# Kernel tuning notes

Hardware: AMD Instinct MI355X
Metric: run time of the kernel (lower is better)

The kernel has to match this reference:

```python
import jax, jax.numpy as jnp
import numpy as np
from jax import lax

B, T, D, H = 256, 512, 128, 256  # batch, seq_len, input_dim, hidden_dim


def _lstm_layer(x_seq, Wih, Whh, bih, bhh):
    """Single PyTorch-convention LSTM layer. x_seq: [B,T,Din] -> [B,T,H].
    Gate order i, f, g, o; h0 = c0 = 0."""
    Bsz = x_seq.shape[0]
    Hd = Whh.shape[1]
    # Precompute input contributions for all timesteps: [B,T,4H]
    xg = jnp.einsum('btd,gd->btg', x_seq, Wih) + bih + bhh

    def step(carry, xg_t):
        h, c = carry
        gates = xg_t + h @ Whh.T  # [B,4H]
        i, f, g, o = jnp.split(gates, 4, axis=-1)
        i = jax.nn.sigmoid(i)
        f = jax.nn.sigmoid(f)
        g = jnp.tanh(g)
        o = jax.nn.sigmoid(o)
        c = f * c + i * g
        h = o * jnp.tanh(c)
        return (h, c), h

    init = (jnp.zeros((Bsz, Hd), x_seq.dtype), jnp.zeros((Bsz, Hd), x_seq.dtype))
    _, hs = lax.scan(step, init, jnp.swapaxes(xg, 0, 1))  # hs: [T,B,H]
    return jnp.swapaxes(hs, 0, 1)


def setup_inputs() -> dict:
    key = jax.random.key(0)
    ks = jax.random.split(key, 12)
    x = jax.random.normal(ks[0], (B, T, D), dtype=jnp.float32)
    # Left-contiguous mask: lengths in [1, T] (pack_padded_sequence semantics)
    lengths = jax.random.randint(ks[1], (B,), 1, T + 1)
    mask = (jnp.arange(T)[None, :] < lengths[:, None]).astype(jnp.int32)
    s0 = 1.0 / np.sqrt(H)
    u = lambda k, shape: jax.random.uniform(k, shape, jnp.float32, -s0, s0)
    return {
        'x': x,
        'mask': mask,
        'W_ih0': u(ks[2], (4 * H, D)),
        'W_hh0': u(ks[3], (4 * H, H)),
        'b_ih0': u(ks[4], (4 * H,)),
        'b_hh0': u(ks[5], (4 * H,)),
        'W_ih1': u(ks[6], (4 * H, H)),
        'W_hh1': u(ks[7], (4 * H, H)),
        'b_ih1': u(ks[8], (4 * H,)),
        'b_hh1': u(ks[9], (4 * H,)),
        'fc_w': u(ks[10], (1, H)),
        'fc_b': u(ks[11], (1,)),
    }


def reference(x, mask, W_ih0, W_hh0, b_ih0, b_hh0, W_ih1, W_hh1, b_ih1, b_hh1, fc_w, fc_b):
    # 2-layer LSTM (dropout inactive at inference)
    h1 = _lstm_layer(x, W_ih0, W_hh0, b_ih0, b_hh0)   # [B,T,H]
    h2 = _lstm_layer(h1, W_ih1, W_hh1, b_ih1, b_hh1)  # [B,T,H]
    # Gather output at last valid timestep per sequence (== packed result)
    lens = jnp.sum(mask, axis=1)                      # [B]
    last = h2[jnp.arange(h2.shape[0]), lens - 1]      # [B,H]
    return last @ fc_w.T + fc_b                       # [B,1]
```

## Files before the change

### kernel.cpp

```cpp
#include <hip/hip_runtime.h>
#include <stdint.h>

#define B_ 256
#define T_ 512
#define D_ 128
#define H_ 256

typedef __attribute__((ext_vector_type(8))) _Float16 half8;
typedef __attribute__((ext_vector_type(4))) float f32x4;
typedef __attribute__((ext_vector_type(4))) int i32x4;

#define WS_PART 0
#define WS_H0   65536
#define WS_H1   (WS_H0 + 2*B_*H_*4)
#define WS_F0   (WS_H1 + 2*B_*H_*4)
#define WS_F1   (WS_F0 + 2*B_*H_*4)

__device__ __forceinline__ float fast_sig(float x) {
    return 1.0f / (1.0f + __expf(-x));
}
__device__ __forceinline__ float fast_tanh(float x) {
    float xc = fminf(fmaxf(x, -30.0f), 30.0f);
    float e = __expf(-2.0f * xc);
    return (1.0f - e) / (1.0f + e);
}
__device__ __forceinline__ half8 cvt8(const float* p) {
    const f32x4* q = (const f32x4*)p;
    f32x4 a = q[0], b = q[1];
    half8 r;
    r[0] = (_Float16)a[0]; r[1] = (_Float16)a[1];
    r[2] = (_Float16)a[2]; r[3] = (_Float16)a[3];
    r[4] = (_Float16)b[0]; r[5] = (_Float16)b[1];
    r[6] = (_Float16)b[2]; r[7] = (_Float16)b[3];
    return r;
}
__device__ __forceinline__ half8 cvt8v(f32x4 a, f32x4 b) {
    half8 r;
    r[0] = (_Float16)a[0]; r[1] = (_Float16)a[1];
    r[2] = (_Float16)a[2]; r[3] = (_Float16)a[3];
    r[4] = (_Float16)b[0]; r[5] = (_Float16)b[1];
    r[6] = (_Float16)b[2]; r[7] = (_Float16)b[3];
    return r;
}

__device__ __forceinline__ void bar_lds() {
    asm volatile("s_waitcnt lgkmcnt(0)" ::: "memory");
    __builtin_amdgcn_s_barrier();
}

__device__ __forceinline__ void poll4f_issue(const unsigned* p, i32x4* r) {
    asm volatile(
        "global_load_dwordx4 %0, %4, off sc0\n\t"
        "global_load_dwordx4 %1, %4, off offset:16 sc0\n\t"
        "global_load_dwordx4 %2, %4, off offset:128 sc0\n\t"
        "global_load_dwordx4 %3, %4, off offset:144 sc0"
        : "=&v"(r[0]), "=&v"(r[1]), "=&v"(r[2]), "=&v"(r[3])
        : "v"(p) : "memory");
}
__device__ __forceinline__ void poll4f_wait(const unsigned* p, i32x4* r) {
    asm volatile(
        "global_load_dwordx4 %0, %4, off sc0\n\t"
        "global_load_dwordx4 %1, %4, off offset:16 sc0\n\t"
        "global_load_dwordx4 %2, %4, off offset:128 sc0\n\t"
        "global_load_dwordx4 %3, %4, off offset:144 sc0\n\t"
        "s_waitcnt vmcnt(0)"
        : "=&v"(r[0]), "=&v"(r[1]), "=&v"(r[2]), "=&v"(r[3])
        : "v"(p) : "memory");
}
__device__ __forceinline__ void store_dw_l2(unsigned* p, unsigned v) {
    asm volatile("global_store_dword %0, %1, off sc0" :: "v"(p), "v"(v) : "memory");
}

__device__ __forceinline__ void poll4_wait(const unsigned* p, i32x4* r) {
    asm volatile(
        "global_load_dwordx4 %0, %4, off sc0 sc1\n\t"
        "global_load_dwordx4 %1, %4, off offset:16 sc0 sc1\n\t"
        "global_load_dwordx4 %2, %4, off offset:128 sc0 sc1\n\t"
        "global_load_dwordx4 %3, %4, off offset:144 sc0 sc1\n\t"
        "s_waitcnt vmcnt(0)"
        : "=&v"(r[0]), "=&v"(r[1]), "=&v"(r[2]), "=&v"(r[3])
        : "v"(p) : "memory");
}
__device__ __forceinline__ void store_dw_mall(unsigned* p, unsigned v) {
    asm volatile("global_store_dword %0, %1, off sc0 sc1" :: "v"(p), "v"(v) : "memory");
}

__device__ __forceinline__ void wait_tie8_vm2(i32x4* a, i32x4* b) {
    asm volatile("s_waitcnt vmcnt(2)"
        : "+v"(a[0]), "+v"(a[1]), "+v"(a[2]), "+v"(a[3]),
          "+v"(b[0]), "+v"(b[1]), "+v"(b[2]), "+v"(b[3]) :: "memory");
}

__device__ __forceinline__ int tags_ok(const i32x4* r, unsigned tag) {
    unsigned m = 0;
#pragma unroll
    for (int i = 0; i < 4; ++i) {
        m |= ((unsigned)r[i][0] ^ tag); m |= ((unsigned)r[i][1] ^ tag);
        m |= ((unsigned)r[i][2] ^ tag); m |= ((unsigned)r[i][3] ^ tag);
    }
    return __all((m & 0xFFFF0000u) == 0);
}
__device__ __forceinline__ void unpack_to_lds(const i32x4* r, _Float16* base) {
#pragma unroll
    for (int t = 0; t < 2; ++t) {
        i32x4 pk;
        pk[0] = (r[2 * t][0] & 0xFFFF) | (r[2 * t][1] << 16);
        pk[1] = (r[2 * t][2] & 0xFFFF) | (r[2 * t][3] << 16);
        pk[2] = (r[2 * t + 1][0] & 0xFFFF) | (r[2 * t + 1][1] << 16);
        pk[3] = (r[2 * t + 1][2] & 0xFFFF) | (r[2 * t + 1][3] << 16);
        *(i32x4*)(base + t * 32) = pk;
    }
}

__global__ __launch_bounds__(256, 1) void lstm_main(
    const float* __restrict__ x, const int* __restrict__ mask,
    const float* __restrict__ Wih0, const float* __restrict__ Whh0,
    const float* __restrict__ bih0, const float* __restrict__ bhh0,
    const float* __restrict__ Wih1, const float* __restrict__ Whh1,
    const float* __restrict__ bih1, const float* __restrict__ bhh1,
    const float* __restrict__ fcw, char* __restrict__ ws)
{
    const int tid  = threadIdx.x;
    const int blk  = blockIdx.x;
    const int g    = blk & 15;
    const int sl   = blk >> 4;
    const int b0   = g * 16;
    const int j0   = sl * 16;
    const int w    = tid >> 6;
    const int lane = tid & 63;
    const int row  = lane & 15;
    const int quad = lane >> 4;
    const int kb   = quad * 8;

    float*    partials = (float*)(ws + WS_PART);
    unsigned* h0u      = (unsigned*)(ws + WS_H0);
    unsigned* h1u      = (unsigned*)(ws + WS_H1);
    unsigned* f0u      = (unsigned*)(ws + WS_F0);
    unsigned* f1u      = (unsigned*)(ws + WS_F1);

    __shared__ float gbuf[2048];
    __shared__ __align__(16) _Float16 hsh0[16 * 264];
    __shared__ __align__(16) _Float16 hsh1[16 * 264];

    const int n = w * H_ + j0 + row;
    half8 wA[12], wB[16];
#pragma unroll
    for (int kt = 0; kt < 4; ++kt) wA[kt]     = cvt8(&Wih0[(size_t)n * D_ + kt * 32 + kb]);
#pragma unroll
    for (int kt = 0; kt < 8; ++kt) wA[4 + kt] = cvt8(&Whh0[(size_t)n * H_ + kt * 32 + kb]);
#pragma unroll
    for (int kt = 0; kt < 8; ++kt) wB[kt]     = cvt8(&Wih1[(size_t)n * H_ + kt * 32 + kb]);
#pragma unroll
    for (int kt = 0; kt < 8; ++kt) wB[8 + kt] = cvt8(&Whh1[(size_t)n * H_ + kt * 32 + kb]);
    const float biasA = bih0[n] + bhh0[n];
    const float biasB = bih1[n] + bhh1[n];

    const int bb    = tid >> 4;
    const int jj    = tid & 15;
    const int bglob = b0 + bb;

    int len = 0;
    {
        const int* mrow = mask + (size_t)bglob * T_ + jj * 32;
#pragma unroll
        for (int q = 0; q < 32; ++q) len += mrow[q];
#pragma unroll
        for (int o = 1; o < 16; o <<= 1) len += __shfl_xor(len, o, 16);
    }

    float c0 = 0.f, c1 = 0.f, hsave = 0.f;

    const float* xrow = x + (size_t)(b0 + row) * T_ * D_ + kb;
    f32x4 xacc = {0.f, 0.f, 0.f, 0.f};
#pragma unroll
    for (int kt = 0; kt < 4; ++kt)
        xacc = __builtin_amdgcn_mfma_f32_16x16x32_f16(cvt8(xrow + kt * 32), wA[kt], xacc, 0, 0, 0);

    i32x4 r0[4], r1[4];
    const int koff = w * 64 + quad * 8;

    for (int u = 0; u <= T_; ++u) {
        half8 a0[8], a1[8];
        f32x4 xr[8];
        int h1ok = 1;
        const unsigned tag1 = (unsigned)(u - 1) << 16;
        const size_t off1 = ((size_t)(u & 1) * B_ + (b0 + row)) * H_ + koff;
        unsigned pv0 = 0, pv1 = 0;
        size_t   so0 = 0, so1 = 0;

        if (u >= 1) {
            wait_tie8_vm2(r0, r1);
            const unsigned tag0 = (unsigned)u << 16;
            const size_t off0 = ((size_t)((u - 1) & 1) * B_ + (b0 + row)) * H_ + koff;
            if (!tags_ok(r0, tag0)) {
                poll4f_wait(f0u + off0, r0);
                int guard = 0;
                while (!tags_ok(r0, tag0)) {
                    poll4_wait(h0u + off0, r0);
                    if (++guard > (1 << 16)) break;
                }
            }
            h1ok = (u >= 2) ? tags_ok(r1, tag1) : 1;
            {
                const int tn = (u + 1 < T_) ? (u + 1) : (T_ - 1);
                const f32x4* q = (const f32x4*)(xrow + (size_t)tn * D_);
#pragma unroll
                for (int kt = 0; kt < 4; ++kt) { xr[2 * kt] = q[kt * 8]; xr[2 * kt + 1] = q[kt * 8 + 1]; }
            }
            unpack_to_lds(r0, hsh0 + row * 264 + koff);
            bar_lds();
#pragma unroll
            for (int kt = 0; kt < 8; ++kt)
                a0[kt] = *(const half8*)(hsh0 + row * 264 + kt * 32 + quad * 8);
        } else {
            const f32x4* q = (const f32x4*)(xrow + (size_t)1 * D_);
#pragma unroll
            for (int kt = 0; kt < 4; ++kt) { xr[2 * kt] = q[kt * 8]; xr[2 * kt + 1] = q[kt * 8 + 1]; }
        }

        if (u < T_) {
            f32x4 acc0 = xacc;
            if (u >= 1) {
#pragma unroll
                for (int kt = 0; kt < 8; ++kt)
                    acc0 = __builtin_amdgcn_mfma_f32_16x16x32_f16(a0[kt], wA[4 + kt], acc0, 0, 0, 0);
            }
#pragma unroll
            for (int r = 0; r < 4; ++r)
                gbuf[w * 256 + (quad * 4 + r) * 16 + row] = acc0[r] + biasA;
            bar_lds();
            const int idx = bb * 16 + jj;
            float gi = fast_sig(gbuf[idx]);
            float gf = fast_sig(gbuf[256 + idx]);
            float gg = fast_tanh(gbuf[512 + idx]);
            float go = fast_sig(gbuf[768 + idx]);
            c0 = gf * c0 + gi * gg;
            float h0v = go * fast_tanh(c0);
            union { _Float16 h; unsigned short s; } cv; cv.h = (_Float16)h0v;
            pv0 = ((unsigned)(u + 1) << 16) | cv.s;
            so0 = ((size_t)(u & 1) * B_ + bglob) * H_ + j0 + jj;
            store_dw_l2(f0u + so0, pv0);
        }
        __builtin_amdgcn_sched_barrier(0);

        if (u >= 1) {
            f32x4 acc1 = {0.f, 0.f, 0.f, 0.f};
#pragma unroll
            for (int kt = 0; kt < 8; ++kt)
                acc1 = __builtin_amdgcn_mfma_f32_16x16x32_f16(a0[kt], wB[kt], acc1, 0, 0, 0);
            if (u >= 2) {
                if (!h1ok) {
                    poll4f_wait(f1u + off1, r1);
                    h1ok = tags_ok(r1, tag1);
                    int guard = 0;
                    while (!h1ok) {
                        poll4_wait(h1u + off1, r1);
                        h1ok = tags_ok(r1, tag1);
                        if (++guard > (1 << 16)) break;
                    }
                }
                unpack_to_lds(r1, hsh1 + row * 264 + koff);
                bar_lds();
#pragma unroll
                for (int kt = 0; kt < 8; ++kt)
                    a1[kt] = *(const half8*)(hsh1 + row * 264 + kt * 32 + quad * 8);
#pragma unroll
                for (int kt = 0; kt < 8; ++kt)
                    acc1 = __builtin_amdgcn_mfma_f32_16x16x32_f16(a1[kt], wB[8 + kt], acc1, 0, 0, 0);
            }
#pragma unroll
            for (int r = 0; r < 4; ++r)
                gbuf[1024 + w * 256 + (quad * 4 + r) * 16 + row] = acc1[r] + biasB;
            bar_lds();
            const int idx = bb * 16 + jj;
            float gi = fast_sig(gbuf[1024 + idx]);
            float gf = fast_sig(gbuf[1024 + 256 + idx]);
            float gg = fast_tanh(gbuf[1024 + 512 + idx]);
            float go = fast_sig(gbuf[1024 + 768 + idx]);
            c1 = gf * c1 + gi * gg;
            float h1v = go * fast_tanh(c1);
            union { _Float16 h; unsigned short s; } cv; cv.h = (_Float16)h1v;
            pv1 = ((unsigned)u << 16) | cv.s;
            so1 = ((size_t)((u - 1) & 1) * B_ + bglob) * H_ + j0 + jj;
            store_dw_l2(f1u + so1, pv1);
            if (u == len) hsave = h1v;
        }

        if (u < T_) {
            const int v = u + 1;
            const unsigned* q0 = f0u + ((size_t)((v - 1) & 1) * B_ + (b0 + row)) * H_ + koff;
            const unsigned* q1 = (v >= 2)
                ? f1u + ((size_t)(v & 1) * B_ + (b0 + row)) * H_ + koff
                : q0;
            poll4f_issue(q0, r0);
            poll4f_issue(q1, r1);
        }

        if (u < T_ - 1) {
            f32x4 t = {0.f, 0.f, 0.f, 0.f};
#pragma unroll
            for (int kt = 0; kt < 4; ++kt)
                t = __builtin_amdgcn_mfma_f32_16x16x32_f16(cvt8v(xr[2 * kt], xr[2 * kt + 1]), wA[kt], t, 0, 0, 0);
            xacc = t;
        }
        __builtin_amdgcn_sched_barrier(0);

        if (u < T_)  store_dw_mall(h0u + so0, pv0);
        if (u >= 1)  store_dw_mall(h1u + so1, pv1);
    }

    float part = hsave * fcw[j0 + jj];
#pragma unroll
    for (int o = 1; o < 16; o <<= 1) part += __shfl_xor(part, o, 16);
    if (jj == 0) partials[sl * B_ + bglob] = part;
}

__global__ void lstm_fc(const float* __restrict__ fcb, const char* __restrict__ ws,
                        float* __restrict__ out) {
    const int b = threadIdx.x;
    const float* partials = (const float*)(ws + WS_PART);
    float s = fcb[0];
#pragma unroll
    for (int sl = 0; sl < 16; ++sl) s += partials[sl * B_ + b];
    out[b] = s;
}

extern "C" void kernel_launch(void* const* d_in, const int* in_sizes, int n_in,
                              void* d_out, int out_size, void* d_ws, size_t ws_size,
                              hipStream_t stream) {
    const float* xx    = (const float*)d_in[0];
    const int*   mask  = (const int*)d_in[1];
    const float* Wih0  = (const float*)d_in[2];
    const float* Whh0  = (const float*)d_in[3];
    const float* bih0  = (const float*)d_in[4];
    const float* bhh0  = (const float*)d_in[5];
    const float* Wih1  = (const float*)d_in[6];
    const float* Whh1  = (const float*)d_in[7];
    const float* bih1  = (const float*)d_in[8];
    const float* bhh1  = (const float*)d_in[9];
    const float* fcw   = (const float*)d_in[10];
    const float* fcb   = (const float*)d_in[11];

    lstm_main<<<dim3(256), dim3(256), 0, stream>>>(
        xx, mask, Wih0, Whh0, bih0, bhh0, Wih1, Whh1, bih1, bhh1, fcw, (char*)d_ws);
    lstm_fc<<<dim3(1), dim3(256), 0, stream>>>(fcb, (const char*)d_ws, (float*)d_out);
}
```

Baseline: 1.760 ms.

## Interleave gate rows per wave and transpose gates via shuffles instead of LDS

Permutes the weight rows each wave owns so the four gates (i,f,g,o) of the same hidden unit land in adjacent lanes of one MFMA output tile. Gate activations are then exchanged with two xor-shuffles, which removes the gbuf LDS round-trip and one block barrier per layer per timestep. The MFMA chains are also split into two independent accumulators to shorten dependency latency, and the polling loop now alternates between the fast and MALL buffers. The final FC reduction is reorganised through a small shared array, and tanh is now computed as 2*sigmoid(2x)-1.

```diff
diff --git a/kernel.cpp b/kernel.cpp
--- a/kernel.cpp
+++ b/kernel.cpp
@@ -110,6 +110,25 @@
         pk[3] = (r[2 * t + 1][2] & 0xFFFF) | (r[2 * t + 1][3] << 16);
         *(i32x4*)(base + t * 32) = pk;
     }
+}
+
+__device__ __forceinline__ void gates_transpose(float* zv, int gsel, float bias) {
+    const float sc = (gsel == 2) ? 2.0f : 1.0f;
+#pragma unroll
+    for (int t = 0; t < 4; ++t) {
+        float y = fast_sig(sc * (zv[t] + bias));
+        zv[t] = (gsel == 2) ? (2.0f * y - 1.0f) : y;
+    }
+    float s0 = (gsel & 1) ? zv[0] : zv[1];
+    float s1 = (gsel & 1) ? zv[2] : zv[3];
+    float r0 = __shfl_xor(s0, 1);
+    float r1 = __shfl_xor(s1, 1);
+    if (gsel & 1) { zv[0] = r0; zv[2] = r1; } else { zv[1] = r0; zv[3] = r1; }
+    float s2 = (gsel & 2) ? zv[0] : zv[2];
+    float s3 = (gsel & 2) ? zv[1] : zv[3];
+    float r2 = __shfl_xor(s2, 2);
+    float r3 = __shfl_xor(s3, 2);
+    if (gsel & 2) { zv[0] = r2; zv[1] = r3; } else { zv[2] = r2; zv[3] = r3; }
 }
 
 __global__ __launch_bounds__(256, 1) void lstm_main(
@@ -131,6 +150,10 @@
     const int row  = lane & 15;
     const int quad = lane >> 4;
     const int kb   = quad * 8;
+    const int gsel = lane & 3;
+    const int jl   = (lane >> 2) & 3;
+    const int bl   = quad * 4 + gsel;
+    const int jglob = j0 + w * 4 + jl;
 
     float*    partials = (float*)(ws + WS_PART);
     unsigned* h0u      = (unsigned*)(ws + WS_H0);
@@ -138,11 +161,11 @@
     unsigned* f0u      = (unsigned*)(ws + WS_F0);
     unsigned* f1u      = (unsigned*)(ws + WS_F1);
 
-    __shared__ float gbuf[2048];
     __shared__ __align__(16) _Float16 hsh0[16 * 264];
     __shared__ __align__(16) _Float16 hsh1[16 * 264];
-
-    const int n = w * H_ + j0 + row;
+    __shared__ float sred[4][16];
+
+    const int n = (row & 3) * H_ + j0 + w * 4 + (row >> 2);
     half8 wA[12], wB[16];
 #pragma unroll
     for (int kt = 0; kt < 4; ++kt) wA[kt]     = cvt8(&Wih0[(size_t)n * D_ + kt * 32 + kb]);
@@ -155,17 +178,16 @@
     const float biasA = bih0[n] + bhh0[n];
     const float biasB = bih1[n] + bhh1[n];
 
-    const int bb    = tid >> 4;
-    const int jj    = tid & 15;
-    const int bglob = b0 + bb;
-
     int len = 0;
     {
-        const int* mrow = mask + (size_t)bglob * T_ + jj * 32;
-#pragma unroll
-        for (int q = 0; q < 32; ++q) len += mrow[q];
-#pragma unroll
-        for (int o = 1; o < 16; o <<= 1) len += __shfl_xor(len, o, 16);
+        const int* mrow = mask + (size_t)(b0 + bl) * T_ + jl * 128;
+#pragma unroll
+        for (int q = 0; q < 32; ++q) {
+            i32x4 m = ((const i32x4*)mrow)[q];
+            len += m[0] + m[1] + m[2] + m[3];
+        }
+        len += __shfl_xor(len, 4);
+        len += __shfl_xor(len, 8);
     }
 
     float c0 = 0.f, c1 = 0.f, hsave = 0.f;
@@ -193,12 +215,12 @@
             const unsigned tag0 = (unsigned)u << 16;
             const size_t off0 = ((size_t)((u - 1) & 1) * B_ + (b0 + row)) * H_ + koff;
             if (!tags_ok(r0, tag0)) {
-                poll4f_wait(f0u + off0, r0);
                 int guard = 0;
-                while (!tags_ok(r0, tag0)) {
-                    poll4_wait(h0u + off0, r0);
+                do {
+                    if (guard < 3 || !(guard & 1)) poll4f_wait(f0u + off0, r0);
+                    else                           poll4_wait(h0u + off0, r0);
                     if (++guard > (1 << 16)) break;
-                }
+                } while (!tags_ok(r0, tag0));
             }
             h1ok = (u >= 2) ? tags_ok(r1, tag1) : 1;
             {
@@ -219,69 +241,66 @@
         }
 
         if (u < T_) {
-            f32x4 acc0 = xacc;
+            f32x4 accA = xacc, accB = {0.f, 0.f, 0.f, 0.f};
             if (u >= 1) {
 #pragma unroll
-                for (int kt = 0; kt < 8; ++kt)
-                    acc0 = __builtin_amdgcn_mfma_f32_16x16x32_f16(a0[kt], wA[4 + kt], acc0, 0, 0, 0);
-            }
-#pragma unroll
-            for (int r = 0; r < 4; ++r)
-                gbuf[w * 256 + (quad * 4 + r) * 16 + row] = acc0[r] + biasA;
-            bar_lds();
-            const int idx = bb * 16 + jj;
-            float gi = fast_sig(gbuf[idx]);
-            float gf = fast_sig(gbuf[256 + idx]);
-            float gg = fast_tanh(gbuf[512 + idx]);
-            float go = fast_sig(gbuf[768 + idx]);
-            c0 = gf * c0 + gi * gg;
-            float h0v = go * fast_tanh(c0);
+                for (int kt = 0; kt < 4; ++kt) {
+                    accA = __builtin_amdgcn_mfma_f32_16x16x32_f16(a0[2 * kt],     wA[4 + 2 * kt],     accA, 0, 0, 0);
+                    accB = __builtin_amdgcn_mfma_f32_16x16x32_f16(a0[2 * kt + 1], wA[4 + 2 * kt + 1], accB, 0, 0, 0);
+                }
+            }
+            float zv[4];
+#pragma unroll
+            for (int t = 0; t < 4; ++t) zv[t] = accA[t] + accB[t];
+            gates_transpose(zv, gsel, biasA);
+            c0 = zv[1] * c0 + zv[0] * zv[2];
+            float h0v = zv[3] * fast_tanh(c0);
             union { _Float16 h; unsigned short s; } cv; cv.h = (_Float16)h0v;
             pv0 = ((unsigned)(u + 1) << 16) | cv.s;
-            so0 = ((size_t)(u & 1) * B_ + bglob) * H_ + j0 + jj;
+            so0 = ((size_t)(u & 1) * B_ + (b0 + bl)) * H_ + jglob;
             store_dw_l2(f0u + so0, pv0);
         }
         __builtin_amdgcn_sched_barrier(0);
 
         if (u >= 1) {
-            f32x4 acc1 = {0.f, 0.f, 0.f, 0.f};
-#pragma unroll
-            for (int kt = 0; kt < 8; ++kt)
-                acc1 = __builtin_amdgcn_mfma_f32_16x16x32_f16(a0[kt], wB[kt], acc1, 0, 0, 0);
+            f32x4 acc1a = {0.f, 0.f, 0.f, 0.f}, acc1b = {0.f, 0.f, 0.f, 0.f};
+#pragma unroll
+            for (int kt = 0; kt < 4; ++kt) {
+                acc1a = __builtin_amdgcn_mfma_f32_16x16x32_f16(a0[2 * kt],     wB[2 * kt],     acc1a, 0, 0, 0);
+                acc1b = __builtin_amdgcn_mfma_f32_16x16x32_f16(a0[2 * kt + 1], wB[2 * kt + 1], acc1b, 0, 0, 0);
+            }
             if (u >= 2) {
                 if (!h1ok) {
-                    poll4f_wait(f1u + off1, r1);
-                    h1ok = tags_ok(r1, tag1);
                     int guard = 0;
-                    while (!h1ok) {
-                        poll4_wait(h1u + off1, r1);
+                    do {
+                        if (guard < 3 || !(guard & 1)) poll4f_wait(f1u + off1, r1);
+                        else                           poll4_wait(h1u + off1, r1);
                         h1ok = tags_ok(r1, tag1);
                         if (++guard > (1 << 16)) break;
-                    }
+                    } while (!h1ok);
                 }
                 unpack_to_lds(r1, hsh1 + row * 264 + koff);
-                bar_lds();
+            }
+            bar_lds();
+            if (u >= 2) {
 #pragma unroll
                 for (int kt = 0; kt < 8; ++kt)
                     a1[kt] = *(const half8*)(hsh1 + row * 264 + kt * 32 + quad * 8);
 #pragma unroll
-                for (int kt = 0; kt < 8; ++kt)
-                    acc1 = __builtin_amdgcn_mfma_f32_16x16x32_f16(a1[kt], wB[8 + kt], acc1, 0, 0, 0);
-            }
-#pragma unroll
-            for (int r = 0; r < 4; ++r)
-                gbuf[1024 + w * 256 + (quad * 4 + r) * 16 + row] = acc1[r] + biasB;
-            bar_lds();
-            const int idx = bb * 16 + jj;
-            float gi = fast_sig(gbuf[1024 + idx]);
-            float gf = fast_sig(gbuf[1024 + 256 + idx]);
-            float gg = fast_tanh(gbuf[1024 + 512 + idx]);
-            float go = fast_sig(gbuf[1024 + 768 + idx]);
-            c1 = gf * c1 + gi * gg;
-            float h1v = go * fast_tanh(c1);
+                for (int kt = 0; kt < 4; ++kt) {
+                    acc1a = __builtin_amdgcn_mfma_f32_16x16x32_f16(a1[2 * kt],     wB[8 + 2 * kt],     acc1a, 0, 0, 0);
+                    acc1b = __builtin_amdgcn_mfma_f32_16x16x32_f16(a1[2 * kt + 1], wB[8 + 2 * kt + 1], acc1b, 0, 0, 0);
+                }
+            }
+            float zv[4];
+#pragma unroll
+            for (int t = 0; t < 4; ++t) zv[t] = acc1a[t] + acc1b[t];
+            gates_transpose(zv, gsel, biasB);
+            c1 = zv[1] * c1 + zv[0] * zv[2];
+            float h1v = zv[3] * fast_tanh(c1);
             union { _Float16 h; unsigned short s; } cv; cv.h = (_Float16)h1v;
             pv1 = ((unsigned)u << 16) | cv.s;
-            so1 = ((size_t)((u - 1) & 1) * B_ + bglob) * H_ + j0 + jj;
+            so1 = ((size_t)((u - 1) & 1) * B_ + (b0 + bl)) * H_ + jglob;
             store_dw_l2(f1u + so1, pv1);
             if (u == len) hsave = h1v;
         }
@@ -309,10 +328,13 @@
         if (u >= 1)  store_dw_mall(h1u + so1, pv1);
     }
 
-    float part = hsave * fcw[j0 + jj];
-#pragma unroll
-    for (int o = 1; o < 16; o <<= 1) part += __shfl_xor(part, o, 16);
-    if (jj == 0) partials[sl * B_ + bglob] = part;
+    float part = hsave * fcw[jglob];
+    part += __shfl_xor(part, 4);
+    part += __shfl_xor(part, 8);
+    if (jl == 0) sred[w][bl] = part;
+    __syncthreads();
+    if (tid < 16)
+        partials[sl * B_ + b0 + tid] = sred[0][tid] + sred[1][tid] + sred[2][tid] + sred[3][tid];
 }
 
 __global__ void lstm_fc(const float* __restrict__ fcb, const char* __restrict__ ws,
```

Measured after the change: 1.840 ms. +4.5%, slower.
